# Kernel tuning notes

Hardware: AMD Instinct MI355X
Metric: run time of the kernel (lower is better)

## Reference

```python
import jax, jax.numpy as jnp
import numpy as np

WINDOW = 2  # window_size

def _causal_window_conv(x, W, b):
    # x: [B,T,D_in], W: [WINDOW, D_in, D_out], b: [D_out]
    # equivalent to left-padding x by WINDOW-1 zeros and a 'valid' conv
    B, T, _ = x.shape
    xp = jnp.pad(x, ((0, 0), (WINDOW - 1, 0), (0, 0)))  # [B, T+WINDOW-1, D_in]
    out = b
    for k in range(WINDOW):
        out = out + jnp.einsum('btd,de->bte', xp[:, k:k + T], W[k])
    return out  # [B,T,D_out]

def setup_inputs() -> dict:
    key = jax.random.key(0)
    ks = jax.random.split(key, 4)
    B, T, Din, Dout = 8, 4096, 256, 256
    scale = 0.05
    x = jax.random.normal(ks[0], (B, T, Din), dtype=jnp.float32)
    W_z = jax.random.normal(ks[1], (WINDOW, Din, Dout), dtype=jnp.float32) * scale
    W_f = jax.random.normal(ks[2], (WINDOW, Din, Dout), dtype=jnp.float32) * scale
    W_o = jax.random.normal(ks[3], (WINDOW, Din, Dout), dtype=jnp.float32) * scale
    b_z = jnp.zeros((Dout,), dtype=jnp.float32)
    b_f = jnp.zeros((Dout,), dtype=jnp.float32)
    b_o = jnp.zeros((Dout,), dtype=jnp.float32)
    return {"x": x, "W_z": W_z, "W_f": W_f, "W_o": W_o,
            "b_z": b_z, "b_f": b_f, "b_o": b_o}

def reference(x, W_z, W_f, W_o, b_z, b_f, b_o):
    # QRNN with fo-pooling (Bradbury et al. 2016), return_sequences=True
    z = jnp.tanh(_causal_window_conv(x, W_z, b_z))          # [B,T,D]
    f = jax.nn.sigmoid(_causal_window_conv(x, W_f, b_f))    # [B,T,D]
    o = jax.nn.sigmoid(_causal_window_conv(x, W_o, b_o))    # [B,T,D]

    def step(c, zfo):
        z_t, f_t, o_t = zfo
        c = f_t * c + (1.0 - f_t) * z_t   # fo-pooling recurrence
        h = o_t * c
        return c, h

    c0 = jnp.zeros(z.shape[::2], dtype=z.dtype)  # [B,D]
    # time-major for scan
    zfo = (z.transpose(1, 0, 2), f.transpose(1, 0, 2), o.transpose(1, 0, 2))
    _, hs = jax.lax.scan(step, c0, zfo)
    return hs.transpose(1, 0, 2)  # [B,T,D]
```

## Files before the change

### kernel.cpp

```cpp
#include <hip/hip_runtime.h>
#include <hip/hip_bf16.h>
#include <hip/hip_fp16.h>

#define BDIM 8
#define TDIM 4096
#define DDIM 256
#define MDIM (BDIM * TDIM)
#define NCHUNK 256
#define LCHUNK (TDIM / NCHUNK)

typedef _Float16 f16x8 __attribute__((ext_vector_type(8)));
typedef _Float16 f16x4 __attribute__((ext_vector_type(4)));
typedef float f32x4 __attribute__((ext_vector_type(4)));

__device__ __forceinline__ float sigmoid_(float x) {
    return 1.0f / (1.0f + __expf(-x));
}
__device__ __forceinline__ float tanh_(float x) {
    return 2.0f / (1.0f + __expf(-2.0f * x)) - 1.0f;
}

#define GLOAD_LDS16(g, l)                                                    \
    __builtin_amdgcn_global_load_lds(                                        \
        (const __attribute__((address_space(1))) void*)(g),                  \
        (__attribute__((address_space(3))) void*)(l), 16, 0, 0)

__global__ __launch_bounds__(64) void convert_x(const float* __restrict__ x,
                                                _Float16* __restrict__ xpad) {
    const int tp = blockIdx.x;
    const int b = blockIdx.y;
    const int q = threadIdx.x;
    float4 v = make_float4(0.f, 0.f, 0.f, 0.f);
    if (tp > 0)
        v = *(const float4*)(x + ((size_t)b * TDIM + tp - 1) * DDIM + q * 4);
    f16x4 h;
    h[0] = (_Float16)v.x; h[1] = (_Float16)v.y;
    h[2] = (_Float16)v.z; h[3] = (_Float16)v.w;
    *(f16x4*)(xpad + ((size_t)b * (TDIM + 1) + tp) * DDIM + q * 4) = h;
}

__global__ __launch_bounds__(256) void convert_w(
    const float* __restrict__ Wz, const float* __restrict__ Wf,
    const float* __restrict__ Wo, _Float16* __restrict__ Wt) {
    const int idx = blockIdx.x * 256 + threadIdx.x;
    const int n = idx & 255;
    const int kin = (idx >> 8) & 255;
    const int w = (idx >> 16) & 1;
    const int g = idx >> 17;
    const float* W = (g == 0) ? Wz : (g == 1) ? Wf : Wo;
    const float v = W[(size_t)w * 65536 + (size_t)kin * 256 + n];
    Wt[((size_t)g * 256 + n) * 512 + w * 256 + kin] = (_Float16)v;
}

__global__ __launch_bounds__(256) void gates_mfma(
    const _Float16* __restrict__ xpad, const _Float16* __restrict__ Wt,
    const float* __restrict__ bz, const float* __restrict__ bfv,
    const float* __restrict__ bo,
    _Float16* __restrict__ zbuf, _Float16* __restrict__ fbuf,
    _Float16* __restrict__ obuf) {
    const int gate = blockIdx.z;
    const int m0 = blockIdx.x * 128;
    const int n0 = blockIdx.y * 128;
    const int tid = threadIdx.x;
    const int lane = tid & 63;
    const int wave = tid >> 6;
    const int wr = wave >> 1;
    const int wc = wave & 1;

    __shared__ __align__(16) char smem[40960];

    const int s = wave * 64 + lane;
    const int r1 = s >> 2;
    const int kc = (s & 3) * 8;

    const int b = m0 >> 12;
    const int t0 = m0 & (TDIM - 1);

    const _Float16* srcA1 =
        xpad + ((size_t)b * (TDIM + 1) + t0 + r1) * DDIM + kc;
    const _Float16* srcA2 = srcA1 + (size_t)64 * DDIM;
    const _Float16* srcB1 = Wt + ((size_t)gate * 256 + n0 + r1) * 512 + kc;
    const _Float16* srcB2 = srcB1 + (size_t)64 * 512;

    f32x4 acc[4][4] = {};
    const int am = lane & 15;
    const int kq = (lane >> 4) * 8;

    {
        char* dA = smem + wave * 1024;
        char* dB = smem + 8192 + wave * 1024;
        GLOAD_LDS16(srcA1, dA);
        GLOAD_LDS16(srcA2, dA + 4096);
        GLOAD_LDS16(srcB1, dB);
        GLOAD_LDS16(srcB2, dB + 4096);
    }

    for (int it = 0; it < 16; ++it) {
        __syncthreads();
        const int cur = it & 1;
        if (it < 15) {
            const int k1 = (it + 1) * 32;
            char* dA = smem + (cur ^ 1) * 16384 + wave * 1024;
            char* dB = smem + (cur ^ 1) * 16384 + 8192 + wave * 1024;
            GLOAD_LDS16(srcA1 + k1, dA);
            GLOAD_LDS16(srcA2 + k1, dA + 4096);
            GLOAD_LDS16(srcB1 + k1, dB);
            GLOAD_LDS16(srcB2 + k1, dB + 4096);
        }
        const _Float16* Ab = (const _Float16*)(smem + cur * 16384);
        const _Float16* Bb = (const _Float16*)(smem + cur * 16384 + 8192);

        f16x8 a[4], bb[4];
#pragma unroll
        for (int i = 0; i < 4; ++i)
            a[i] = *(const f16x8*)(Ab + (wr * 64 + i * 16 + am) * 32 + kq);
#pragma unroll
        for (int j = 0; j < 4; ++j)
            bb[j] = *(const f16x8*)(Bb + (wc * 64 + j * 16 + am) * 32 + kq);
#pragma unroll
        for (int i = 0; i < 4; ++i)
#pragma unroll
            for (int j = 0; j < 4; ++j)
                acc[i][j] = __builtin_amdgcn_mfma_f32_16x16x32_f16(
                    a[i], bb[j], acc[i][j], 0, 0, 0);
    }

    __syncthreads();

    const float* bias = (gate == 0) ? bz : (gate == 1) ? bfv : bo;
    _Float16* outp = (gate == 0) ? zbuf : (gate == 1) ? fbuf : obuf;
    _Float16* eb = (_Float16*)smem + wave * 5120;
    const int rq = (lane >> 4) * 4;
#pragma unroll
    for (int j = 0; j < 4; ++j) {
        const int gc = n0 + wc * 64 + j * 16 + am;
        const float bj = bias[gc];
#pragma unroll
        for (int i = 0; i < 4; ++i) {
            f32x4 v = acc[i][j];
#pragma unroll
            for (int r = 0; r < 4; ++r) {
                const float val = v[r] + bj;
                const float act = (gate == 0) ? tanh_(val) : sigmoid_(val);
                eb[(i * 16 + rq + r) * 80 + j * 16 + am] = (_Float16)act;
            }
        }
    }
    __syncthreads();

    const int rrow = lane >> 3;
    const int rcol = (lane & 7) * 8;
#pragma unroll
    for (int rr = 0; rr < 8; ++rr) {
        const int row = rr * 8 + rrow;
        f16x8 v = *(const f16x8*)(eb + row * 80 + rcol);
        const size_t gm = (size_t)(m0 + wr * 64 + row);
        *(f16x8*)(outp + gm * DDIM + n0 + wc * 64 + rcol) = v;
    }
}

__global__ __launch_bounds__(256) void scan_pass1(
    const _Float16* __restrict__ zbuf, const _Float16* __restrict__ fbuf,
    float* __restrict__ aggA, float* __restrict__ aggB) {
    const int idx = blockIdx.x * 256 + threadIdx.x;
    const int d8 = idx & 31;
    const int chunk = (idx >> 5) & (NCHUNK - 1);
    const int b = idx >> 13;

    const size_t row0 = (size_t)b * TDIM + (size_t)chunk * LCHUNK;
    const int4* zp = (const int4*)zbuf + row0 * 32 + d8;
    const int4* fp = (const int4*)fbuf + row0 * 32 + d8;

    float A[8], c[8];
#pragma unroll
    for (int e = 0; e < 8; ++e) { A[e] = 1.0f; c[e] = 0.0f; }

    for (int i = 0; i < LCHUNK; ++i) {
        int4 fv = *fp;
        int4 zv = *zp;
        const _Float16* fh = (const _Float16*)&fv;
        const _Float16* zh = (const _Float16*)&zv;
#pragma unroll
        for (int e = 0; e < 8; ++e) {
            const float f = (float)fh[e];
            const float z = (float)zh[e];
            A[e] *= f;
            c[e] = f * c[e] + (1.0f - f) * z;
        }
        fp += 32;
        zp += 32;
    }
    ((float4*)aggA)[(size_t)idx * 2 + 0] = make_float4(A[0], A[1], A[2], A[3]);
    ((float4*)aggA)[(size_t)idx * 2 + 1] = make_float4(A[4], A[5], A[6], A[7]);
    ((float4*)aggB)[(size_t)idx * 2 + 0] = make_float4(c[0], c[1], c[2], c[3]);
    ((float4*)aggB)[(size_t)idx * 2 + 1] = make_float4(c[4], c[5], c[6], c[7]);
}

__global__ __launch_bounds__(256) void carry_scan(
    const float* __restrict__ aggA, const float* __restrict__ aggB,
    float* __restrict__ carry) {
    const int g = blockIdx.x * 256 + threadIdx.x;
    const int d = g & 255;
    const int b = g >> 8;
    const size_t base = (size_t)b * NCHUNK * 256 + d;

    float c = 0.0f;
    for (int ch0 = 0; ch0 < NCHUNK; ch0 += 8) {
        float A[8], Bv[8];
#pragma unroll
        for (int u = 0; u < 8; ++u) {
            const size_t p = base + (size_t)(ch0 + u) * 256;
            A[u] = aggA[p];
            Bv[u] = aggB[p];
        }
#pragma unroll
        for (int u = 0; u < 8; ++u) {
            const size_t p = base + (size_t)(ch0 + u) * 256;
            carry[p] = c;
            c = A[u] * c + Bv[u];
        }
    }
}

__global__ __launch_bounds__(256) void scan_pass2(
    const _Float16* __restrict__ zbuf, const _Float16* __restrict__ fbuf,
    const _Float16* __restrict__ obuf, const float* __restrict__ carry,
    float* __restrict__ out) {
    const int idx = blockIdx.x * 256 + threadIdx.x;
    const int d8 = idx & 31;
    const int chunk = (idx >> 5) & (NCHUNK - 1);
    const int b = idx >> 13;

    float c[8];
    float4 c0 = ((const float4*)carry)[(size_t)idx * 2];
    float4 c1 = ((const float4*)carry)[(size_t)idx * 2 + 1];
    c[0] = c0.x; c[1] = c0.y; c[2] = c0.z; c[3] = c0.w;
    c[4] = c1.x; c[5] = c1.y; c[6] = c1.z; c[7] = c1.w;

    const size_t row0 = (size_t)b * TDIM + (size_t)chunk * LCHUNK;
    const int4* zp = (const int4*)zbuf + row0 * 32 + d8;
    const int4* fp = (const int4*)fbuf + row0 * 32 + d8;
    const int4* op = (const int4*)obuf + row0 * 32 + d8;
    float4* hp = (float4*)out + row0 * 64 + d8 * 2;

    for (int i = 0; i < LCHUNK; ++i) {
        int4 fv = *fp;
        int4 zv = *zp;
        int4 ov = *op;
        const _Float16* fh = (const _Float16*)&fv;
        const _Float16* zh = (const _Float16*)&zv;
        const _Float16* oh = (const _Float16*)&ov;
        float h[8];
#pragma unroll
        for (int e = 0; e < 8; ++e) {
            const float f = (float)fh[e];
            const float z = (float)zh[e];
            c[e] = f * c[e] + (1.0f - f) * z;
            h[e] = (float)oh[e] * c[e];
        }
        hp[0] = make_float4(h[0], h[1], h[2], h[3]);
        hp[1] = make_float4(h[4], h[5], h[6], h[7]);
        fp += 32;
        zp += 32;
        op += 32;
        hp += 64;
    }
}

extern "C" void kernel_launch(void* const* d_in, const int* in_sizes, int n_in,
                              void* d_out, int out_size, void* d_ws,
                              size_t ws_size, hipStream_t stream) {
    const float* x = (const float*)d_in[0];
    const float* Wz = (const float*)d_in[1];
    const float* Wf = (const float*)d_in[2];
    const float* Wo = (const float*)d_in[3];
    const float* bz = (const float*)d_in[4];
    const float* bfv = (const float*)d_in[5];
    const float* bo = (const float*)d_in[6];
    float* out = (float*)d_out;

    char* p = (char*)d_ws;
    _Float16* xpad = (_Float16*)p;  p += (size_t)BDIM * (TDIM + 1) * DDIM * 2;
    _Float16* Wt = (_Float16*)p;    p += (size_t)3 * 256 * 512 * 2;
    _Float16* zbuf = (_Float16*)p;  p += (size_t)MDIM * DDIM * 2;
    _Float16* fbuf = (_Float16*)p;  p += (size_t)MDIM * DDIM * 2;
    _Float16* obuf = (_Float16*)p;  p += (size_t)MDIM * DDIM * 2;
    float* aggA = (float*)p;        p += (size_t)BDIM * NCHUNK * DDIM * 4;
    float* aggB = (float*)p;        p += (size_t)BDIM * NCHUNK * DDIM * 4;
    float* carry = (float*)p;

    convert_x<<<dim3(TDIM + 1, BDIM), 64, 0, stream>>>(x, xpad);
    convert_w<<<(3 * 2 * 256 * 256) / 256, 256, 0, stream>>>(Wz, Wf, Wo, Wt);

    gates_mfma<<<dim3(MDIM / 128, DDIM / 128, 3), 256, 0, stream>>>(
        xpad, Wt, bz, bfv, bo, zbuf, fbuf, obuf);

    scan_pass1<<<(BDIM * NCHUNK * 32) / 256, 256, 0, stream>>>(zbuf, fbuf,
                                                               aggA, aggB);
    carry_scan<<<(BDIM * DDIM) / 256, 256, 0, stream>>>(aggA, aggB, carry);
    scan_pass2<<<(BDIM * NCHUNK * 32) / 256, 256, 0, stream>>>(zbuf, fbuf,
                                                               obuf, carry, out);
}
```

Measured before the change: 174.6 us.

## Fuse fp32-to-fp16 x conversion and causal padding into GEMM tile loads

Drops the separate convert_x kernel and the padded fp16 copy of x. The GEMM now reads fp32 x directly, applies the causal shift and zero padding per tile, converts to fp16 in registers, and stores it to LDS. The direct global-to-LDS async loads are replaced by register-staged loads that are stored after the MFMA block to keep double buffering. It also fully unrolls the scan chunk loops. The trade-off is one kernel launch and one full pass over x saved, against twice the fp32 bytes per A tile, with x re-read across 6 grid blocks (2 N-tiles times 3 gates), plus extra register pressure and conversion ALU work inside the GEMM.

```diff
diff --git a/kernel.cpp b/kernel.cpp
--- a/kernel.cpp
+++ b/kernel.cpp
@@ -20,23 +20,13 @@
     return 2.0f / (1.0f + __expf(-2.0f * x)) - 1.0f;
 }
 
-#define GLOAD_LDS16(g, l)                                                    \
-    __builtin_amdgcn_global_load_lds(                                        \
-        (const __attribute__((address_space(1))) void*)(g),                  \
-        (__attribute__((address_space(3))) void*)(l), 16, 0, 0)
-
-__global__ __launch_bounds__(64) void convert_x(const float* __restrict__ x,
-                                                _Float16* __restrict__ xpad) {
-    const int tp = blockIdx.x;
-    const int b = blockIdx.y;
-    const int q = threadIdx.x;
-    float4 v = make_float4(0.f, 0.f, 0.f, 0.f);
-    if (tp > 0)
-        v = *(const float4*)(x + ((size_t)b * TDIM + tp - 1) * DDIM + q * 4);
-    f16x4 h;
-    h[0] = (_Float16)v.x; h[1] = (_Float16)v.y;
-    h[2] = (_Float16)v.z; h[3] = (_Float16)v.w;
-    *(f16x4*)(xpad + ((size_t)b * (TDIM + 1) + tp) * DDIM + q * 4) = h;
+__device__ __forceinline__ f16x8 cvt8(const float4 a, const float4 b) {
+    f16x8 r;
+    r[0] = (_Float16)a.x; r[1] = (_Float16)a.y;
+    r[2] = (_Float16)a.z; r[3] = (_Float16)a.w;
+    r[4] = (_Float16)b.x; r[5] = (_Float16)b.y;
+    r[6] = (_Float16)b.z; r[7] = (_Float16)b.w;
+    return r;
 }
 
 __global__ __launch_bounds__(256) void convert_w(
@@ -53,7 +43,7 @@
 }
 
 __global__ __launch_bounds__(256) void gates_mfma(
-    const _Float16* __restrict__ xpad, const _Float16* __restrict__ Wt,
+    const float* __restrict__ x, const _Float16* __restrict__ Wt,
     const float* __restrict__ bz, const float* __restrict__ bfv,
     const float* __restrict__ bo,
     _Float16* __restrict__ zbuf, _Float16* __restrict__ fbuf,
@@ -69,44 +59,58 @@
 
     __shared__ __align__(16) char smem[40960];
 
-    const int s = wave * 64 + lane;
-    const int r1 = s >> 2;
-    const int kc = (s & 3) * 8;
+    const int arow = tid >> 1;
+    const int ac = (tid & 1) * 16;
 
     const int b = m0 >> 12;
     const int t0 = m0 & (TDIM - 1);
 
-    const _Float16* srcA1 =
-        xpad + ((size_t)b * (TDIM + 1) + t0 + r1) * DDIM + kc;
-    const _Float16* srcA2 = srcA1 + (size_t)64 * DDIM;
-    const _Float16* srcB1 = Wt + ((size_t)gate * 256 + n0 + r1) * 512 + kc;
-    const _Float16* srcB2 = srcB1 + (size_t)64 * 512;
+    const float* xb = x + (size_t)b * TDIM * DDIM;
+    const _Float16* pB = Wt + ((size_t)gate * 256 + n0 + arow) * 512 + ac;
+
+    float4 ga0, ga1, ga2, ga3;
+    int4 gb0, gb1;
+
+#define LOAD_TILE(k0)                                                        \
+    {                                                                        \
+        const int half = (k0) >> 8;                                          \
+        const int kin = (k0) & 255;                                          \
+        const int t = t0 + arow - 1 + half;                                  \
+        if (t >= 0) {                                                        \
+            const float* src = xb + (size_t)t * DDIM + kin + ac;             \
+            ga0 = *(const float4*)(src);                                     \
+            ga1 = *(const float4*)(src + 4);                                 \
+            ga2 = *(const float4*)(src + 8);                                 \
+            ga3 = *(const float4*)(src + 12);                                \
+        } else {                                                             \
+            ga0 = ga1 = ga2 = ga3 = make_float4(0.f, 0.f, 0.f, 0.f);         \
+        }                                                                    \
+        gb0 = *(const int4*)(pB + (k0));                                     \
+        gb1 = *(const int4*)(pB + (k0) + 8);                                 \
+    }
+
+#define STORE_TILE(bufp)                                                     \
+    {                                                                        \
+        _Float16* Ad = (_Float16*)(bufp);                                    \
+        _Float16* Bd = (_Float16*)((char*)(bufp) + 8192);                    \
+        *(f16x8*)(Ad + arow * 32 + ac) = cvt8(ga0, ga1);                     \
+        *(f16x8*)(Ad + arow * 32 + ac + 8) = cvt8(ga2, ga3);                 \
+        *(int4*)(Bd + arow * 32 + ac) = gb0;                                 \
+        *(int4*)(Bd + arow * 32 + ac + 8) = gb1;                             \
+    }
 
     f32x4 acc[4][4] = {};
     const int am = lane & 15;
     const int kq = (lane >> 4) * 8;
 
-    {
-        char* dA = smem + wave * 1024;
-        char* dB = smem + 8192 + wave * 1024;
-        GLOAD_LDS16(srcA1, dA);
-        GLOAD_LDS16(srcA2, dA + 4096);
-        GLOAD_LDS16(srcB1, dB);
-        GLOAD_LDS16(srcB2, dB + 4096);
-    }
+    LOAD_TILE(0);
+    STORE_TILE(smem);
 
     for (int it = 0; it < 16; ++it) {
         __syncthreads();
         const int cur = it & 1;
-        if (it < 15) {
-            const int k1 = (it + 1) * 32;
-            char* dA = smem + (cur ^ 1) * 16384 + wave * 1024;
-            char* dB = smem + (cur ^ 1) * 16384 + 8192 + wave * 1024;
-            GLOAD_LDS16(srcA1 + k1, dA);
-            GLOAD_LDS16(srcA2 + k1, dA + 4096);
-            GLOAD_LDS16(srcB1 + k1, dB);
-            GLOAD_LDS16(srcB2 + k1, dB + 4096);
-        }
+        if (it < 15) LOAD_TILE((it + 1) * 32);
+
         const _Float16* Ab = (const _Float16*)(smem + cur * 16384);
         const _Float16* Bb = (const _Float16*)(smem + cur * 16384 + 8192);
 
@@ -123,6 +127,8 @@
             for (int j = 0; j < 4; ++j)
                 acc[i][j] = __builtin_amdgcn_mfma_f32_16x16x32_f16(
                     a[i], bb[j], acc[i][j], 0, 0, 0);
+
+        if (it < 15) STORE_TILE(smem + (cur ^ 1) * 16384);
     }
 
     __syncthreads();
@@ -157,6 +163,8 @@
         const size_t gm = (size_t)(m0 + wr * 64 + row);
         *(f16x8*)(outp + gm * DDIM + n0 + wc * 64 + rcol) = v;
     }
+#undef LOAD_TILE
+#undef STORE_TILE
 }
 
 __global__ __launch_bounds__(256) void scan_pass1(
@@ -175,6 +183,7 @@
 #pragma unroll
     for (int e = 0; e < 8; ++e) { A[e] = 1.0f; c[e] = 0.0f; }
 
+#pragma unroll
     for (int i = 0; i < LCHUNK; ++i) {
         int4 fv = *fp;
         int4 zv = *zp;
@@ -243,6 +252,7 @@
     const int4* op = (const int4*)obuf + row0 * 32 + d8;
     float4* hp = (float4*)out + row0 * 64 + d8 * 2;
 
+#pragma unroll
     for (int i = 0; i < LCHUNK; ++i) {
         int4 fv = *fp;
         int4 zv = *zp;
@@ -280,7 +290,6 @@
     float* out = (float*)d_out;
 
     char* p = (char*)d_ws;
-    _Float16* xpad = (_Float16*)p;  p += (size_t)BDIM * (TDIM + 1) * DDIM * 2;
     _Float16* Wt = (_Float16*)p;    p += (size_t)3 * 256 * 512 * 2;
     _Float16* zbuf = (_Float16*)p;  p += (size_t)MDIM * DDIM * 2;
     _Float16* fbuf = (_Float16*)p;  p += (size_t)MDIM * DDIM * 2;
@@ -289,11 +298,10 @@
     float* aggB = (float*)p;        p += (size_t)BDIM * NCHUNK * DDIM * 4;
     float* carry = (float*)p;
 
-    convert_x<<<dim3(TDIM + 1, BDIM), 64, 0, stream>>>(x, xpad);
     convert_w<<<(3 * 2 * 256 * 256) / 256, 256, 0, stream>>>(Wz, Wf, Wo, Wt);
 
     gates_mfma<<<dim3(MDIM / 128, DDIM / 128, 3), 256, 0, stream>>>(
-        xpad, Wt, bz, bfv, bo, zbuf, fbuf, obuf);
+        x, Wt, bz, bfv, bo, zbuf, fbuf, obuf);
 
     scan_pass1<<<(BDIM * NCHUNK * 32) / 256, 256, 0, stream>>>(zbuf, fbuf,
                                                                aggA, aggB);
```

Measured after the change: 181.3 us. 3.8% more time.
